# Kernel optimization log

Measured on AMD Instinct MI355X. Metric: run time of the kernel, lower is better.

## Reference

```python
import jax, jax.numpy as jnp
import numpy as np

N_NODES = 40000
N_EDGES = 1280000
D_FEAT = 1024
HIDDEN = 64
N_CLASSES = 40


def gcn_conv(x, edge_index, W, b):
    # PyG GCNConv: linear transform, add self-loops, symmetric deg^{-1/2} normalization, scatter-add
    n = x.shape[0]
    h = x @ W  # [N, out]
    loop = jnp.arange(n, dtype=edge_index.dtype)
    row = jnp.concatenate([edge_index[0], loop])  # source
    col = jnp.concatenate([edge_index[1], loop])  # target
    deg = jax.ops.segment_sum(jnp.ones_like(col, dtype=x.dtype), col, num_segments=n)
    dinv = jnp.where(deg > 0, jax.lax.rsqrt(deg), 0.0).astype(x.dtype)
    norm = dinv[row] * dinv[col]  # [E+N]
    msg = h[row] * norm[:, None]
    out = jax.ops.segment_sum(msg, col, num_segments=n)
    return out + b


def setup_inputs() -> dict:
    key = jax.random.key(0)
    k1, k2, k3, k4 = jax.random.split(key, 4)
    x = jax.random.normal(k1, (N_NODES, D_FEAT), dtype=jnp.float32)
    edge_index = jax.random.randint(k2, (2, N_EDGES), 0, N_NODES, dtype=jnp.int32)
    W1 = jax.random.normal(k3, (D_FEAT, HIDDEN), dtype=jnp.float32) * (1.0 / np.sqrt(D_FEAT))
    b1 = jnp.zeros((HIDDEN,), dtype=jnp.float32)
    W2 = jax.random.normal(k4, (HIDDEN, N_CLASSES), dtype=jnp.float32) * (1.0 / np.sqrt(HIDDEN))
    b2 = jnp.zeros((N_CLASSES,), dtype=jnp.float32)
    return {"x": x, "edge_index": edge_index, "W1": W1, "b1": b1, "W2": W2, "b2": b2}


def reference(x, edge_index, W1, b1, W2, b2):
    h = gcn_conv(x, edge_index, W1, b1)
    h = jax.nn.relu(h)
    # F.dropout(training=False) -> identity in eval mode
    h = gcn_conv(h, edge_index, W2, b2)
    return jax.nn.log_softmax(h, axis=1)
```

## Files before the change

### kernel.cpp

```cpp
#include <hip/hip_runtime.h>
#include <hip/hip_bf16.h>
#include <math.h>

#define N_NODES 40000
#define N_EDGES 1280000
#define D_FEAT 1024
#define HIDDEN 64
#define N_CLASSES 40
#define NB 157
#define CHUNK 4096

typedef _Float16 f16x8 __attribute__((ext_vector_type(8)));
typedef _Float16 f16x2 __attribute__((ext_vector_type(2)));
typedef float f32x4 __attribute__((ext_vector_type(4)));


#define HIST_BLOCKS 313
#define CONV_BLOCKS 256

__global__ __launch_bounds__(256) void k_pre(const int* __restrict__ col,
                                             int* __restrict__ btot,
                                             const float* __restrict__ W,
                                             _Float16* __restrict__ Wt) {
    __shared__ int h[NB];
    int tid = threadIdx.x;
    if (blockIdx.x < HIST_BLOCKS) {
        if (tid < NB) h[tid] = 0;
        __syncthreads();
        int e0 = blockIdx.x * 4096;
        int e1 = min(e0 + 4096, N_EDGES);
        for (int e = e0 + tid; e < e1; e += 256)
            atomicAdd(&h[col[e] >> 8], 1);
        __syncthreads();
        if (tid < NB && h[tid]) atomicAdd(&btot[tid], h[tid]);
    } else {
        int i = (blockIdx.x - HIST_BLOCKS) * 256 + tid;
        int n = i & 63, k = i >> 6;
        Wt[n * D_FEAT + k] = (_Float16)W[k * HIDDEN + n];
    }
}


__global__ __launch_bounds__(256) void k_binscatter(const int* __restrict__ row,
                                                    const int* __restrict__ col,
                                                    const int* __restrict__ btot,
                                                    int* __restrict__ gcur,
                                                    unsigned* __restrict__ sedge) {
    __shared__ unsigned stage[CHUNK];
    __shared__ unsigned char bo[CHUNK];
    __shared__ int sc[256];
    __shared__ int bb[NB];
    __shared__ int hist[NB];
    __shared__ int lo[NB];
    __shared__ int cur[NB];
    __shared__ int dst[NB];
    const int tid = threadIdx.x;
    const int e0 = blockIdx.x * CHUNK;
    const int nE = min(CHUNK, N_EDGES - e0);

    if (tid < NB) { hist[tid] = 0; cur[tid] = 0; }
    int bv = (tid < NB) ? btot[tid] : 0;
    sc[tid] = bv;
    __syncthreads();
#pragma unroll
    for (int d = 1; d < 256; d <<= 1) {
        int t = (tid >= d) ? sc[tid - d] : 0;
        __syncthreads();
        sc[tid] += t;
        __syncthreads();
    }
    if (tid < NB) bb[tid] = sc[tid] - bv;

    int c[16];
#pragma unroll
    for (int t = 0; t < 16; ++t) {
        int e = tid + t * 256;
        c[t] = (e < nE) ? col[e0 + e] : -1;
        if (e < nE) atomicAdd(&hist[c[t] >> 8], 1);
    }
    __syncthreads();

    int hv = (tid < NB) ? hist[tid] : 0;
    sc[tid] = hv;
    __syncthreads();
#pragma unroll
    for (int d = 1; d < 256; d <<= 1) {
        int t = (tid >= d) ? sc[tid - d] : 0;
        __syncthreads();
        sc[tid] += t;
        __syncthreads();
    }
    if (tid < NB) {
        int excl = sc[tid] - hv;
        lo[tid] = excl;
        int cp = hv ? atomicAdd(&gcur[tid], hv) : 0;
        dst[tid] = bb[tid] + cp - excl;
    }
    __syncthreads();

#pragma unroll
    for (int t = 0; t < 16; ++t) {
        int e = tid + t * 256;
        if (e < nE) {
            int b = c[t] >> 8;
            int p = lo[b] + atomicAdd(&cur[b], 1);
            stage[p] = ((unsigned)(c[t] & 255) << 16) | (unsigned)row[e0 + e];
            bo[p] = (unsigned char)b;
        }
    }
    __syncthreads();
    for (int i = tid; i < nE; i += 256)
        sedge[dst[bo[i]] + i] = stage[i];
}


__global__ __launch_bounds__(256) void k_bucketsort(const unsigned* __restrict__ sedge,
                                                    const int* __restrict__ btot,
                                                    int* __restrict__ off,
                                                    float* __restrict__ dinv,
                                                    unsigned short* __restrict__ sorted) {
    __shared__ int sc[256];
    __shared__ int hist[256];
    __shared__ int cur[256];
    const int tid = threadIdx.x;
    const int b = blockIdx.x;
    int bv = (tid < NB) ? btot[tid] : 0;
    sc[tid] = bv;
    hist[tid] = 0;
    __syncthreads();
#pragma unroll
    for (int d = 1; d < 256; d <<= 1) {
        int t = (tid >= d) ? sc[tid - d] : 0;
        __syncthreads();
        sc[tid] += t;
        __syncthreads();
    }
    const int base = (b == 0) ? 0 : sc[b - 1];
    const int end  = sc[b];
    __syncthreads();

    for (int i = base + tid; i < end; i += 256)
        atomicAdd(&hist[sedge[i] >> 16], 1);
    __syncthreads();
    int v = hist[tid];
    sc[tid] = v;
    __syncthreads();
#pragma unroll
    for (int d = 1; d < 256; d <<= 1) {
        int t = (tid >= d) ? sc[tid - d] : 0;
        __syncthreads();
        sc[tid] += t;
        __syncthreads();
    }
    int excl = sc[tid] - v;
    cur[tid] = excl;
    int col0 = b << 8;
    int ncol = min(256, N_NODES - col0);
    if (tid < ncol) {
        off[col0 + tid] = base + excl;
        dinv[col0 + tid] = rsqrtf((float)(v + 1));
    }
    if (b == NB - 1 && tid == 0) off[N_NODES] = N_EDGES;
    __syncthreads();
    for (int i = base + tid; i < end; i += 256) {
        unsigned e = sedge[i];
        int p = atomicAdd(&cur[e >> 16], 1);
        sorted[base + p] = (unsigned short)e;
    }
}


#define LDA 72
#define LDB 72

__global__ __launch_bounds__(256) void k_gemm1(const float* __restrict__ X,
                                               const _Float16* __restrict__ Wt,
                                               const float* __restrict__ dinv,
                                               _Float16* __restrict__ out) {
    __shared__ _Float16 As[32 * LDA];
    __shared__ _Float16 Bs[64 * LDB];
    const int tid = threadIdx.x;
    const int wave = tid >> 6, lane = tid & 63;
    const int row0 = blockIdx.x * 32;
    const int m0 = (wave & 1) * 16, n0 = (wave >> 1) * 32;
    const int lr = lane & 15, quad = lane >> 4;

    const int ar = tid >> 3;
    const int ak = (tid & 7) * 8;
    const int bn = tid >> 2;
    const int bk = (tid & 3) * 16;

    f32x4 acc0 = {0.f,0.f,0.f,0.f}, acc1 = {0.f,0.f,0.f,0.f};

    for (int k0 = 0; k0 < D_FEAT; k0 += 64) {
        const float* xp = &X[(row0 + ar) * D_FEAT + k0 + ak];
        float4 v0 = *(const float4*)(xp + 0);
        float4 v1 = *(const float4*)(xp + 4);
        f16x8 p0 = {(_Float16)v0.x,(_Float16)v0.y,(_Float16)v0.z,(_Float16)v0.w,
                    (_Float16)v1.x,(_Float16)v1.y,(_Float16)v1.z,(_Float16)v1.w};
        *(f16x8*)&As[ar * LDA + ak] = p0;
        const uint4* wp = (const uint4*)&Wt[bn * D_FEAT + k0 + bk];
        uint4 w0 = wp[0], w1 = wp[1];
        *(uint4*)&Bs[bn * LDB + bk]     = w0;
        *(uint4*)&Bs[bn * LDB + bk + 8] = w1;
        __syncthreads();
#pragma unroll
        for (int kk = 0; kk < 64; kk += 32) {
            f16x8 a  = *(f16x8*)&As[(m0 + lr) * LDA + kk + quad * 8];
            f16x8 b0 = *(f16x8*)&Bs[(n0 + lr) * LDB + kk + quad * 8];
            f16x8 b1 = *(f16x8*)&Bs[(n0 + 16 + lr) * LDB + kk + quad * 8];
            acc0 = __builtin_amdgcn_mfma_f32_16x16x32_f16(a, b0, acc0, 0, 0, 0);
            acc1 = __builtin_amdgcn_mfma_f32_16x16x32_f16(a, b1, acc1, 0, 0, 0);
        }
        __syncthreads();
    }

#pragma unroll
    for (int r = 0; r < 4; ++r) {
        int m = row0 + m0 + quad * 4 + r;
        float dv = dinv[m];
        out[m * HIDDEN + n0 + lr]      = (_Float16)(acc0[r] * dv);
        out[m * HIDDEN + n0 + 16 + lr] = (_Float16)(acc1[r] * dv);
    }
}


__global__ __launch_bounds__(256) void k_g1g2(const int* __restrict__ off,
                                              const unsigned short* __restrict__ sorted,
                                              const _Float16* __restrict__ hs,
                                              const float* __restrict__ dinv,
                                              const float* __restrict__ bias,
                                              const float* __restrict__ W2,
                                              _Float16* __restrict__ B3) {
    __shared__ float W2t[N_CLASSES][65];
    __shared__ float a1s[4][64];
    const int tid = threadIdx.x;
    const int wave = tid >> 6, lane = tid & 63;
    const int node = blockIdx.x * 4 + wave;

    for (int i = tid; i < HIDDEN * N_CLASSES; i += 256)
        W2t[i % N_CLASSES][i / N_CLASSES] = W2[i];

    int h = lane >> 5, fl = lane & 31;
    float ax = 0.f, ay = 0.f;
    if (h == 0) {
        f16x2 v = *(const f16x2*)&hs[node * HIDDEN + 2 * fl];
        ax = (float)v.x; ay = (float)v.y;
    }
    int beg = off[node], end = off[node + 1];
    for (int base = beg; base < end; base += 64) {
        int m = end - base; if (m > 64) m = 64;
        int vidx = (lane < m) ? (int)sorted[base + lane] : 0;
        int i = h;
        for (; i + 6 < m; i += 8) {
            int s0 = __shfl(vidx, i,     64);
            int s1 = __shfl(vidx, i + 2, 64);
            int s2 = __shfl(vidx, i + 4, 64);
            int s3 = __shfl(vidx, i + 6, 64);
            f16x2 v0 = *(const f16x2*)&hs[s0 * HIDDEN + 2 * fl];
            f16x2 v1 = *(const f16x2*)&hs[s1 * HIDDEN + 2 * fl];
            f16x2 v2 = *(const f16x2*)&hs[s2 * HIDDEN + 2 * fl];
            f16x2 v3 = *(const f16x2*)&hs[s3 * HIDDEN + 2 * fl];
            ax += (float)v0.x + (float)v1.x + (float)v2.x + (float)v3.x;
            ay += (float)v0.y + (float)v1.y + (float)v2.y + (float)v3.y;
        }
        for (; i < m; i += 2) {
            int s = __shfl(vidx, i, 64);
            f16x2 v = *(const f16x2*)&hs[s * HIDDEN + 2 * fl];
            ax += (float)v.x; ay += (float)v.y;
        }
    }
    ax += __shfl_xor(ax, 32, 64);
    ay += __shfl_xor(ay, 32, 64);
    float dv = dinv[node];
    if (h == 0) {
        float2 o;
        o.x = fmaxf(fmaf(dv, ax, bias[2 * fl + 0]), 0.f);
        o.y = fmaxf(fmaf(dv, ay, bias[2 * fl + 1]), 0.f);
        *(float2*)&a1s[wave][2 * fl] = o;
    }
    __syncthreads();

    if (lane < N_CLASSES) {
        float acc = 0.f;
#pragma unroll
        for (int k = 0; k < HIDDEN; ++k)
            acc = fmaf(a1s[wave][k], W2t[lane][k], acc);
        B3[node * N_CLASSES + lane] = (_Float16)(acc * dv);
    }
}


__global__ __launch_bounds__(256) void k_gather2_lsm(const int* __restrict__ off,
                                                     const unsigned short* __restrict__ sorted,
                                                     const _Float16* __restrict__ hs,
                                                     const float* __restrict__ dinv,
                                                     const float* __restrict__ bias,
                                                     float* __restrict__ out) {
    int node = (blockIdx.x * 256 + threadIdx.x) >> 6;
    int lane = threadIdx.x & 63;
    if (node >= N_NODES) return;
    int h = lane >> 5, fl = lane & 31;
    bool act = fl < 20;
    float ax = 0.f, ay = 0.f;
    if (h == 0 && act) {
        f16x2 v = *(const f16x2*)&hs[node * N_CLASSES + 2 * fl];
        ax = (float)v.x; ay = (float)v.y;
    }
    int beg = off[node], end = off[node + 1];
    for (int base = beg; base < end; base += 64) {
        int m = end - base; if (m > 64) m = 64;
        int vidx = (lane < m) ? (int)sorted[base + lane] : 0;
        int i = h;
        for (; i + 6 < m; i += 8) {
            int s0 = __shfl(vidx, i,     64);
            int s1 = __shfl(vidx, i + 2, 64);
            int s2 = __shfl(vidx, i + 4, 64);
            int s3 = __shfl(vidx, i + 6, 64);
            if (act) {
                f16x2 v0 = *(const f16x2*)&hs[s0 * N_CLASSES + 2 * fl];
                f16x2 v1 = *(const f16x2*)&hs[s1 * N_CLASSES + 2 * fl];
                f16x2 v2 = *(const f16x2*)&hs[s2 * N_CLASSES + 2 * fl];
                f16x2 v3 = *(const f16x2*)&hs[s3 * N_CLASSES + 2 * fl];
                ax += (float)v0.x + (float)v1.x + (float)v2.x + (float)v3.x;
                ay += (float)v0.y + (float)v1.y + (float)v2.y + (float)v3.y;
            }
        }
        for (; i < m; i += 2) {
            int s = __shfl(vidx, i, 64);
            if (act) {
                f16x2 v = *(const f16x2*)&hs[s * N_CLASSES + 2 * fl];
                ax += (float)v.x; ay += (float)v.y;
            }
        }
    }
    ax += __shfl_xor(ax, 32, 64);
    ay += __shfl_xor(ay, 32, 64);
    float dv = dinv[node];
    float zx = act ? fmaf(dv, ax, bias[2 * fl + 0]) : -INFINITY;
    float zy = act ? fmaf(dv, ay, bias[2 * fl + 1]) : -INFINITY;
    float m = fmaxf(zx, zy);
#pragma unroll
    for (int d = 16; d > 0; d >>= 1) m = fmaxf(m, __shfl_xor(m, d, 64));
    float ex = act ? (expf(zx - m) + expf(zy - m)) : 0.f;
#pragma unroll
    for (int d = 16; d > 0; d >>= 1) ex += __shfl_xor(ex, d, 64);
    float lse = m + logf(ex);
    if (h == 0 && act) {
        float2 o; o.x = zx - lse; o.y = zy - lse;
        *(float2*)&out[node * N_CLASSES + 2 * fl] = o;
    }
}


extern "C" void kernel_launch(void* const* d_in, const int* in_sizes, int n_in,
                              void* d_out, int out_size, void* d_ws, size_t ws_size,
                              hipStream_t stream) {
    const float* x  = (const float*)d_in[0];
    const int*   ei = (const int*)d_in[1];
    const float* W1 = (const float*)d_in[2];
    const float* b1 = (const float*)d_in[3];
    const float* W2 = (const float*)d_in[4];
    const float* b2 = (const float*)d_in[5];
    const int* row = ei;
    const int* col = ei + N_EDGES;

    char* ws = (char*)d_ws;
    int*            btot   = (int*)(ws + 0);
    int*            gcur   = (int*)(ws + 1024);
    int*            off    = (int*)(ws + 4096);
    float*          dinv   = (float*)(ws + 167936);
    unsigned*       sedge  = (unsigned*)(ws + 335872);
    unsigned short* sorted = (unsigned short*)(ws + 5455872);
    _Float16*       W1t    = (_Float16*)(ws + 8015872);
    _Float16*       B1     = (_Float16*)(ws + 8146944);
    _Float16*       B3     = (_Float16*)(ws + 13266944);

    hipMemsetAsync(btot, 0, 2048, stream);
    k_pre<<<HIST_BLOCKS + CONV_BLOCKS, 256, 0, stream>>>(col, btot, W1, W1t);
    k_binscatter<<<(N_EDGES + CHUNK - 1) / CHUNK, 256, 0, stream>>>(row, col, btot, gcur, sedge);
    k_bucketsort<<<NB, 256, 0, stream>>>(sedge, btot, off, dinv, sorted);

    k_gemm1<<<N_NODES / 32, 256, 0, stream>>>(x, W1t, dinv, B1);
    k_g1g2<<<N_NODES / 4, 256, 0, stream>>>(off, sorted, B1, dinv, b1, W2, B3);
    k_gather2_lsm<<<(N_NODES + 3) / 4, 256, 0, stream>>>(off, sorted, B3, dinv, b2, (float*)d_out);
}
```

Before: 386.7 us.

## Aggregate before second linear transform and widen gather loads to 16 bytes

The second GCN layer is reordered so it aggregates the 64-wide hidden activations first and applies W2 afterwards, fused with log-softmax. The old order projected to 40 classes and then gathered 40-wide rows. Both gather kernels now read 16-byte f16x8 chunks, with 8 lanes covering one row and 8 neighbours handled at once, instead of f16x2 per lane. This trades a gather over 64-wide rows instead of 40-wide ones for fewer, wider memory transactions and no intermediate B3 buffer. The layer-1 output A1 reuses the sedge workspace region, which is no longer needed at that point.

```diff
diff --git a/kernel.cpp b/kernel.cpp
--- a/kernel.cpp
+++ b/kernel.cpp
@@ -11,7 +11,6 @@
 #define CHUNK 4096
 
 typedef _Float16 f16x8 __attribute__((ext_vector_type(8)));
-typedef _Float16 f16x2 __attribute__((ext_vector_type(2)));
 typedef float f32x4 __attribute__((ext_vector_type(4)));
 
 
@@ -225,131 +224,157 @@
 }
 
 
-__global__ __launch_bounds__(256) void k_g1g2(const int* __restrict__ off,
+__global__ __launch_bounds__(256) void k_agg1(const int* __restrict__ off,
                                               const unsigned short* __restrict__ sorted,
                                               const _Float16* __restrict__ hs,
                                               const float* __restrict__ dinv,
                                               const float* __restrict__ bias,
-                                              const float* __restrict__ W2,
-                                              _Float16* __restrict__ B3) {
-    __shared__ float W2t[N_CLASSES][65];
-    __shared__ float a1s[4][64];
+                                              _Float16* __restrict__ A1) {
     const int tid = threadIdx.x;
     const int wave = tid >> 6, lane = tid & 63;
     const int node = blockIdx.x * 4 + wave;
-
-    for (int i = tid; i < HIDDEN * N_CLASSES; i += 256)
-        W2t[i % N_CLASSES][i / N_CLASSES] = W2[i];
-
-    int h = lane >> 5, fl = lane & 31;
-    float ax = 0.f, ay = 0.f;
-    if (h == 0) {
-        f16x2 v = *(const f16x2*)&hs[node * HIDDEN + 2 * fl];
-        ax = (float)v.x; ay = (float)v.y;
-    }
-    int beg = off[node], end = off[node + 1];
+    const int g = lane >> 3;
+    const int sl = lane & 7;
+
+    float acc[8];
+#pragma unroll
+    for (int j = 0; j < 8; ++j) acc[j] = 0.f;
+    if (g == 0) {
+        f16x8 v = *(const f16x8*)&hs[node * HIDDEN + sl * 8];
+#pragma unroll
+        for (int j = 0; j < 8; ++j) acc[j] = (float)v[j];
+    }
+
+    const int beg = off[node], end = off[node + 1];
     for (int base = beg; base < end; base += 64) {
         int m = end - base; if (m > 64) m = 64;
         int vidx = (lane < m) ? (int)sorted[base + lane] : 0;
-        int i = h;
-        for (; i + 6 < m; i += 8) {
-            int s0 = __shfl(vidx, i,     64);
-            int s1 = __shfl(vidx, i + 2, 64);
-            int s2 = __shfl(vidx, i + 4, 64);
-            int s3 = __shfl(vidx, i + 6, 64);
-            f16x2 v0 = *(const f16x2*)&hs[s0 * HIDDEN + 2 * fl];
-            f16x2 v1 = *(const f16x2*)&hs[s1 * HIDDEN + 2 * fl];
-            f16x2 v2 = *(const f16x2*)&hs[s2 * HIDDEN + 2 * fl];
-            f16x2 v3 = *(const f16x2*)&hs[s3 * HIDDEN + 2 * fl];
-            ax += (float)v0.x + (float)v1.x + (float)v2.x + (float)v3.x;
-            ay += (float)v0.y + (float)v1.y + (float)v2.y + (float)v3.y;
-        }
-        for (; i < m; i += 2) {
-            int s = __shfl(vidx, i, 64);
-            f16x2 v = *(const f16x2*)&hs[s * HIDDEN + 2 * fl];
-            ax += (float)v.x; ay += (float)v.y;
-        }
-    }
-    ax += __shfl_xor(ax, 32, 64);
-    ay += __shfl_xor(ay, 32, 64);
-    float dv = dinv[node];
-    if (h == 0) {
-        float2 o;
-        o.x = fmaxf(fmaf(dv, ax, bias[2 * fl + 0]), 0.f);
-        o.y = fmaxf(fmaf(dv, ay, bias[2 * fl + 1]), 0.f);
-        *(float2*)&a1s[wave][2 * fl] = o;
-    }
-    __syncthreads();
-
-    if (lane < N_CLASSES) {
-        float acc = 0.f;
-#pragma unroll
-        for (int k = 0; k < HIDDEN; ++k)
-            acc = fmaf(a1s[wave][k], W2t[lane][k], acc);
-        B3[node * N_CLASSES + lane] = (_Float16)(acc * dv);
-    }
-}
-
-
-__global__ __launch_bounds__(256) void k_gather2_lsm(const int* __restrict__ off,
-                                                     const unsigned short* __restrict__ sorted,
-                                                     const _Float16* __restrict__ hs,
-                                                     const float* __restrict__ dinv,
-                                                     const float* __restrict__ bias,
-                                                     float* __restrict__ out) {
-    int node = (blockIdx.x * 256 + threadIdx.x) >> 6;
-    int lane = threadIdx.x & 63;
-    if (node >= N_NODES) return;
-    int h = lane >> 5, fl = lane & 31;
-    bool act = fl < 20;
-    float ax = 0.f, ay = 0.f;
-    if (h == 0 && act) {
-        f16x2 v = *(const f16x2*)&hs[node * N_CLASSES + 2 * fl];
-        ax = (float)v.x; ay = (float)v.y;
-    }
-    int beg = off[node], end = off[node + 1];
+        int nfull = m & ~15;
+        int i = 0;
+        for (; i < nfull; i += 16) {
+            int s0 = __shfl(vidx, i + g, 64);
+            int s1 = __shfl(vidx, i + 8 + g, 64);
+            f16x8 v0 = *(const f16x8*)&hs[s0 * HIDDEN + sl * 8];
+            f16x8 v1 = *(const f16x8*)&hs[s1 * HIDDEN + sl * 8];
+#pragma unroll
+            for (int j = 0; j < 8; ++j)
+                acc[j] += (float)v0[j] + (float)v1[j];
+        }
+        if (i < m) {
+            int s0 = __shfl(vidx, i + g, 64);
+            int s1 = __shfl(vidx, i + 8 + g, 64);
+            f16x8 v0 = {};
+            f16x8 v1 = {};
+            if (i + g < m)     v0 = *(const f16x8*)&hs[s0 * HIDDEN + sl * 8];
+            if (i + 8 + g < m) v1 = *(const f16x8*)&hs[s1 * HIDDEN + sl * 8];
+#pragma unroll
+            for (int j = 0; j < 8; ++j)
+                acc[j] += (float)v0[j] + (float)v1[j];
+        }
+    }
+
+#pragma unroll
+    for (int j = 0; j < 8; ++j) {
+        acc[j] += __shfl_xor(acc[j], 8, 64);
+        acc[j] += __shfl_xor(acc[j], 16, 64);
+        acc[j] += __shfl_xor(acc[j], 32, 64);
+    }
+    if (lane < 8) {
+        float dv = dinv[node];
+        f16x8 o;
+#pragma unroll
+        for (int j = 0; j < 8; ++j) {
+            float z = fmaf(dv, acc[j], bias[lane * 8 + j]);
+            o[j] = (_Float16)(fmaxf(z, 0.f) * dv);
+        }
+        *(f16x8*)&A1[node * HIDDEN + lane * 8] = o;
+    }
+}
+
+
+__global__ __launch_bounds__(256) void k_agg2_lsm(const int* __restrict__ off,
+                                                  const unsigned short* __restrict__ sorted,
+                                                  const _Float16* __restrict__ A1,
+                                                  const float* __restrict__ dinv,
+                                                  const float* __restrict__ b2,
+                                                  const float* __restrict__ W2,
+                                                  float* __restrict__ out) {
+    __shared__ float W2s[HIDDEN * N_CLASSES];
+    __shared__ float aggs[4][HIDDEN];
+    const int tid = threadIdx.x;
+    for (int i = tid; i < HIDDEN * N_CLASSES; i += 256) W2s[i] = W2[i];
+    const int wave = tid >> 6, lane = tid & 63;
+    const int node = blockIdx.x * 4 + wave;
+    const int g = lane >> 3, sl = lane & 7;
+
+    float acc[8];
+#pragma unroll
+    for (int j = 0; j < 8; ++j) acc[j] = 0.f;
+    if (g == 0) {
+        f16x8 v = *(const f16x8*)&A1[node * HIDDEN + sl * 8];
+#pragma unroll
+        for (int j = 0; j < 8; ++j) acc[j] = (float)v[j];
+    }
+    __syncthreads();
+
+    const int beg = off[node], end = off[node + 1];
     for (int base = beg; base < end; base += 64) {
         int m = end - base; if (m > 64) m = 64;
         int vidx = (lane < m) ? (int)sorted[base + lane] : 0;
-        int i = h;
-        for (; i + 6 < m; i += 8) {
-            int s0 = __shfl(vidx, i,     64);
-            int s1 = __shfl(vidx, i + 2, 64);
-            int s2 = __shfl(vidx, i + 4, 64);
-            int s3 = __shfl(vidx, i + 6, 64);
-            if (act) {
-                f16x2 v0 = *(const f16x2*)&hs[s0 * N_CLASSES + 2 * fl];
-                f16x2 v1 = *(const f16x2*)&hs[s1 * N_CLASSES + 2 * fl];
-                f16x2 v2 = *(const f16x2*)&hs[s2 * N_CLASSES + 2 * fl];
-                f16x2 v3 = *(const f16x2*)&hs[s3 * N_CLASSES + 2 * fl];
-                ax += (float)v0.x + (float)v1.x + (float)v2.x + (float)v3.x;
-                ay += (float)v0.y + (float)v1.y + (float)v2.y + (float)v3.y;
-            }
-        }
-        for (; i < m; i += 2) {
-            int s = __shfl(vidx, i, 64);
-            if (act) {
-                f16x2 v = *(const f16x2*)&hs[s * N_CLASSES + 2 * fl];
-                ax += (float)v.x; ay += (float)v.y;
-            }
-        }
-    }
-    ax += __shfl_xor(ax, 32, 64);
-    ay += __shfl_xor(ay, 32, 64);
-    float dv = dinv[node];
-    float zx = act ? fmaf(dv, ax, bias[2 * fl + 0]) : -INFINITY;
-    float zy = act ? fmaf(dv, ay, bias[2 * fl + 1]) : -INFINITY;
-    float m = fmaxf(zx, zy);
-#pragma unroll
-    for (int d = 16; d > 0; d >>= 1) m = fmaxf(m, __shfl_xor(m, d, 64));
-    float ex = act ? (expf(zx - m) + expf(zy - m)) : 0.f;
-#pragma unroll
-    for (int d = 16; d > 0; d >>= 1) ex += __shfl_xor(ex, d, 64);
-    float lse = m + logf(ex);
-    if (h == 0 && act) {
-        float2 o; o.x = zx - lse; o.y = zy - lse;
-        *(float2*)&out[node * N_CLASSES + 2 * fl] = o;
-    }
+        int nfull = m & ~15;
+        int i = 0;
+        for (; i < nfull; i += 16) {
+            int s0 = __shfl(vidx, i + g, 64);
+            int s1 = __shfl(vidx, i + 8 + g, 64);
+            f16x8 v0 = *(const f16x8*)&A1[s0 * HIDDEN + sl * 8];
+            f16x8 v1 = *(const f16x8*)&A1[s1 * HIDDEN + sl * 8];
+#pragma unroll
+            for (int j = 0; j < 8; ++j)
+                acc[j] += (float)v0[j] + (float)v1[j];
+        }
+        if (i < m) {
+            int s0 = __shfl(vidx, i + g, 64);
+            int s1 = __shfl(vidx, i + 8 + g, 64);
+            f16x8 v0 = {};
+            f16x8 v1 = {};
+            if (i + g < m)     v0 = *(const f16x8*)&A1[s0 * HIDDEN + sl * 8];
+            if (i + 8 + g < m) v1 = *(const f16x8*)&A1[s1 * HIDDEN + sl * 8];
+#pragma unroll
+            for (int j = 0; j < 8; ++j)
+                acc[j] += (float)v0[j] + (float)v1[j];
+        }
+    }
+#pragma unroll
+    for (int j = 0; j < 8; ++j) {
+        acc[j] += __shfl_xor(acc[j], 8, 64);
+        acc[j] += __shfl_xor(acc[j], 16, 64);
+        acc[j] += __shfl_xor(acc[j], 32, 64);
+    }
+    if (lane < 8) {
+        f32x4 t0 = {acc[0], acc[1], acc[2], acc[3]};
+        f32x4 t1 = {acc[4], acc[5], acc[6], acc[7]};
+        *(f32x4*)&aggs[wave][lane * 8]     = t0;
+        *(f32x4*)&aggs[wave][lane * 8 + 4] = t1;
+    }
+    __builtin_amdgcn_wave_barrier();
+
+    float z = -INFINITY;
+    if (lane < N_CLASSES) {
+        float s = 0.f;
+        const float* ag = aggs[wave];
+#pragma unroll
+        for (int k = 0; k < HIDDEN; ++k)
+            s = fmaf(ag[k], W2s[k * N_CLASSES + lane], s);
+        z = fmaf(dinv[node], s, b2[lane]);
+    }
+    float mv = z;
+#pragma unroll
+    for (int d = 32; d > 0; d >>= 1) mv = fmaxf(mv, __shfl_xor(mv, d, 64));
+    float ex = (lane < N_CLASSES) ? expf(z - mv) : 0.f;
+#pragma unroll
+    for (int d = 32; d > 0; d >>= 1) ex += __shfl_xor(ex, d, 64);
+    float lse = mv + logf(ex);
+    if (lane < N_CLASSES) out[node * N_CLASSES + lane] = z - lse;
 }
 
 
@@ -374,7 +399,7 @@
     unsigned short* sorted = (unsigned short*)(ws + 5455872);
     _Float16*       W1t    = (_Float16*)(ws + 8015872);
     _Float16*       B1     = (_Float16*)(ws + 8146944);
-    _Float16*       B3     = (_Float16*)(ws + 13266944);
+    _Float16*       A1     = (_Float16*)(ws + 335872);
 
     hipMemsetAsync(btot, 0, 2048, stream);
     k_pre<<<HIST_BLOCKS + CONV_BLOCKS, 256, 0, stream>>>(col, btot, W1, W1t);
@@ -382,6 +407,6 @@
     k_bucketsort<<<NB, 256, 0, stream>>>(sedge, btot, off, dinv, sorted);
 
     k_gemm1<<<N_NODES / 32, 256, 0, stream>>>(x, W1t, dinv, B1);
-    k_g1g2<<<N_NODES / 4, 256, 0, stream>>>(off, sorted, B1, dinv, b1, W2, B3);
-    k_gather2_lsm<<<(N_NODES + 3) / 4, 256, 0, stream>>>(off, sorted, B3, dinv, b2, (float*)d_out);
-}
+    k_agg1<<<N_NODES / 4, 256, 0, stream>>>(off, sorted, B1, dinv, b1, A1);
+    k_agg2_lsm<<<N_NODES / 4, 256, 0, stream>>>(off, sorted, A1, dinv, b2, W2, (float*)d_out);
+}
```

New measurement: 384.5 us. Within noise of the previous version (-0.5%).
